# Performance work log

Measured on AMD Instinct MI355X. Metric: run time of the kernel, lower is better.

## Reference

```python
import jax, jax.numpy as jnp
import numpy as np
from jax import lax

C_IN, C_OUT, H, W = 64, 128, 512, 512


def setup_inputs() -> dict:
    key = jax.random.key(0)
    k1, k2, k3, k4 = jax.random.split(key, 4)
    x = jax.random.normal(k1, (C_IN, H, W), dtype=jnp.float32)
    # Conv2d params (eqx default: kernel 3x3, bias used). Small init scale for stability.
    conv_w = jax.random.normal(k2, (C_OUT, C_IN, 3, 3), dtype=jnp.float32) * 0.05
    conv_b = jax.random.normal(k3, (C_OUT,), dtype=jnp.float32) * 0.05
    fft_mask = jax.random.normal(k4, (C_OUT, H, W), dtype=jnp.float32)
    return {"x": x, "conv_w": conv_w, "conv_b": conv_b, "fft_mask": fft_mask}


def reference(x, conv_w, conv_b, fft_mask):
    # 3x3 same-padding conv on a single (C,H,W) sample -> (C_OUT,H,W)
    y = lax.conv_general_dilated(
        x[None],  # (1,C_IN,H,W)
        conv_w,
        window_strides=(1, 1),
        padding=((1, 1), (1, 1)),
        dimension_numbers=("NCHW", "OIHW", "NCHW"),
    )[0] + conv_b[:, None, None]
    # Per-channel spectral filter: FFT over (H,W), elementwise complex-mask
    # multiply, inverse FFT, take real part. Vectorized over channels.
    Y = jnp.fft.fftn(y, axes=(1, 2)) * fft_mask
    return jnp.fft.ifftn(Y, axes=(1, 2)).real
```

## Files before the change

### kernel.cpp

```cpp
#include <hip/hip_runtime.h>

#define CIN   64
#define COUT  128
#define HH    512
#define WW    512
#define HW    (HH*WW)

typedef __attribute__((ext_vector_type(8))) short  short8;
typedef __attribute__((ext_vector_type(4))) float  floatx4;


__device__ __forceinline__ unsigned short f2bf(float f) {
    unsigned u = __float_as_uint(f);
    u += 0x7fffu + ((u >> 16) & 1u);
    return (unsigned short)(u >> 16);
}


__global__ __launch_bounds__(256) void k_wprep(
        const float* __restrict__ cw,
        unsigned short* __restrict__ wt)
{
    int i = blockIdx.x * 256 + threadIdx.x;
    int tap = i >> 13;
    int co  = (i >> 6) & 127;
    int ci  = i & 63;
    wt[i] = f2bf(cw[(co * 64 + ci) * 9 + tap]);
}


__global__ __launch_bounds__(256) void k_xprep(
        const float* __restrict__ x,
        unsigned short* __restrict__ xt)
{
    __shared__ unsigned short tile[64][72];
    int t  = threadIdx.x;
    int h  = blockIdx.x >> 3;
    int w0 = (blockIdx.x & 7) << 6;
    int wl = t & 63;
#pragma unroll
    for (int it = 0; it < 16; ++it) {
        int ci = (t >> 6) + 4 * it;
        tile[wl][ci] = f2bf(x[ci * HW + h * 512 + w0 + wl]);
    }
    __syncthreads();
#pragma unroll
    for (int it = 0; it < 2; ++it) {
        int task = t + 256 * it;
        int w = task >> 3, seg = task & 7;
        *(short8*)&xt[((size_t)(h * 512 + w0 + w)) * 64 + seg * 8] =
            *(const short8*)&tile[w][seg * 8];
    }
}


__global__ __launch_bounds__(512) void k_conv(
        const unsigned short* __restrict__ xt,
        const unsigned short* __restrict__ wt,
        const float* __restrict__ bias,
        float* __restrict__ y)
{
    __shared__ __align__(16) unsigned short As[3][130][68];

    int b  = blockIdx.x;
    int h  = b >> 2;
    int w0 = (b & 3) << 7;
    int t  = threadIdx.x;
    int lane = t & 63, wv = t >> 6;
    int wm = wv >> 2, wn = wv & 3;
    int l15 = lane & 15, quad = lane >> 4;

    for (int idx = t; idx < 3 * 130 * 8; idx += 512) {
        int dy  = idx / 1040;
        int rem = idx - dy * 1040;
        int p   = rem >> 3, seg = rem & 7;
        int hp  = h + dy - 1;
        int wq  = w0 - 1 + p;
        short8 v = {0, 0, 0, 0, 0, 0, 0, 0};
        if ((unsigned)hp < 512u && (unsigned)wq < 512u)
            v = *(const short8*)&xt[((size_t)(hp * 512 + wq)) * 64 + seg * 8];
        *(short8*)&As[dy][p][seg * 8] = v;
    }
    __syncthreads();

    floatx4 acc[4][2];
#pragma unroll
    for (int mt = 0; mt < 4; ++mt)
#pragma unroll
        for (int nt = 0; nt < 2; ++nt) {
            floatx4 z = {0.f, 0.f, 0.f, 0.f};
            acc[mt][nt] = z;
        }

#pragma unroll
    for (int tap = 0; tap < 9; ++tap) {
        int dy = tap / 3, dx = tap - dy * 3;
        short8 bfr[2][2];
#pragma unroll
        for (int nt = 0; nt < 2; ++nt)
#pragma unroll
            for (int kc = 0; kc < 2; ++kc) {
                int co = wn * 32 + nt * 16 + l15;
                bfr[nt][kc] = *(const short8*)
                    &wt[(tap * 128 + co) * 64 + kc * 32 + quad * 8];
            }
#pragma unroll
        for (int kc = 0; kc < 2; ++kc) {
            int c0 = kc * 32 + quad * 8;
            short8 afr[4];
#pragma unroll
            for (int mt = 0; mt < 4; ++mt) {
                int row = wm * 64 + mt * 16 + l15 + dx;
                afr[mt] = *(const short8*)&As[dy][row][c0];
            }
#pragma unroll
            for (int mt = 0; mt < 4; ++mt)
#pragma unroll
                for (int nt = 0; nt < 2; ++nt)
                    acc[mt][nt] = __builtin_amdgcn_mfma_f32_16x16x32_bf16(
                        afr[mt], bfr[nt][kc], acc[mt][nt], 0, 0, 0);
        }
    }

#pragma unroll
    for (int nt = 0; nt < 2; ++nt) {
        int co = wn * 32 + nt * 16 + l15;
        float bv = bias[co];
#pragma unroll
        for (int mt = 0; mt < 4; ++mt) {
            floatx4 o = acc[mt][nt];
            o[0] += bv; o[1] += bv; o[2] += bv; o[3] += bv;
            int m = wm * 64 + mt * 16 + quad * 4;
            *(floatx4*)&y[co * HW + h * 512 + w0 + m] = o;
        }
    }
}


#define FS 576

template<int MODE>
__device__ __forceinline__ int slotf(int c, int a) {
    int m = a + (a >> 3);
    return (MODE == 0) ? c * FS + m
                       : m * 16 + c;
}

__device__ __forceinline__ float2 cadd(float2 a, float2 b){ return make_float2(a.x+b.x, a.y+b.y); }
__device__ __forceinline__ float2 csub(float2 a, float2 b){ return make_float2(a.x-b.x, a.y-b.y); }

template<int DIR> __device__ __forceinline__ float2 twmul(float2 a, float2 t){
    return (DIR > 0) ? make_float2(a.x*t.x - a.y*t.y, a.x*t.y + a.y*t.x)
                     : make_float2(a.x*t.x + a.y*t.y, a.y*t.x - a.x*t.y);
}
template<int DIR> __device__ __forceinline__ float2 mulJ(float2 a){
    return (DIR > 0) ? make_float2(a.y, -a.x) : make_float2(-a.y, a.x);
}

#define RSQRT2 0.70710678118654752f

template<int DIR> __device__ __forceinline__ void dft8(float2* x){
    float2 a0 = cadd(x[0], x[4]), b0 = csub(x[0], x[4]);
    float2 a1 = cadd(x[1], x[5]), b1 = csub(x[1], x[5]);
    float2 a2 = cadd(x[2], x[6]), b2 = csub(x[2], x[6]);
    float2 a3 = cadd(x[3], x[7]), b3 = csub(x[3], x[7]);
    b1 = (DIR > 0) ? make_float2((b1.x + b1.y)*RSQRT2, (b1.y - b1.x)*RSQRT2)
                   : make_float2((b1.x - b1.y)*RSQRT2, (b1.y + b1.x)*RSQRT2);
    b2 = mulJ<DIR>(b2);
    b3 = (DIR > 0) ? make_float2((b3.y - b3.x)*RSQRT2, -(b3.x + b3.y)*RSQRT2)
                   : make_float2(-(b3.x + b3.y)*RSQRT2, (b3.x - b3.y)*RSQRT2);
    float2 c0 = cadd(a0, a2), d0 = csub(a0, a2);
    float2 c1 = cadd(a1, a3), d1 = mulJ<DIR>(csub(a1, a3));
    x[0] = cadd(c0, c1); x[4] = csub(c0, c1);
    x[2] = cadd(d0, d1); x[6] = csub(d0, d1);
    float2 e0 = cadd(b0, b2), f0 = csub(b0, b2);
    float2 e1 = cadd(b1, b3), f1 = mulJ<DIR>(csub(b1, b3));
    x[1] = cadd(e0, e1); x[5] = csub(e0, e1);
    x[3] = cadd(f0, f1); x[7] = csub(f0, f1);
}

template<int MODE>
__device__ __forceinline__ void fft512_fwd(float2 X[4][8], float2* buf,
                                           const float2* tw, int w, int c) {
#pragma unroll
    for (int b = 0; b < 4; ++b) {
        dft8<1>(X[b]);
        int g = w + 16*b;
#pragma unroll
        for (int k = 1; k < 8; ++k) X[b][k] = twmul<1>(X[b][k], tw[g*k]);
    }
#pragma unroll
    for (int b = 0; b < 4; ++b) {
        int g = w + 16*b;
#pragma unroll
        for (int k = 0; k < 8; ++k) buf[slotf<MODE>(c, k*64 + g)] = X[b][k];
    }
    __syncthreads();
#pragma unroll
    for (int b = 0; b < 4; ++b) {
        int u = w + 16*b; int bs = (u >> 3)*64 + (u & 7);
#pragma unroll
        for (int g2 = 0; g2 < 8; ++g2) X[b][g2] = buf[slotf<MODE>(c, bs + 8*g2)];
    }
#pragma unroll
    for (int b = 0; b < 4; ++b) {
        dft8<1>(X[b]);
        int g1 = (w + 16*b) & 7;
#pragma unroll
        for (int k = 1; k < 8; ++k) X[b][k] = twmul<1>(X[b][k], tw[8*g1*k]);
    }
    __syncthreads();
#pragma unroll
    for (int b = 0; b < 4; ++b) {
        int u = w + 16*b; int bs = (u >> 3)*64 + (u & 7);
#pragma unroll
        for (int k = 0; k < 8; ++k) buf[slotf<MODE>(c, bs + 8*k)] = X[b][k];
    }
    __syncthreads();
#pragma unroll
    for (int b = 0; b < 4; ++b) {
        int v = w + 16*b;
#pragma unroll
        for (int g1 = 0; g1 < 8; ++g1) X[b][g1] = buf[slotf<MODE>(c, 8*v + g1)];
    }
#pragma unroll
    for (int b = 0; b < 4; ++b) dft8<1>(X[b]);
}

template<int MODE>
__device__ __forceinline__ void fft512_inv(float2 X[4][8], float2* buf,
                                           const float2* tw, int w, int c) {
#pragma unroll
    for (int b = 0; b < 4; ++b) dft8<-1>(X[b]);
    __syncthreads();
#pragma unroll
    for (int b = 0; b < 4; ++b) {
        int v = w + 16*b;
#pragma unroll
        for (int g1 = 0; g1 < 8; ++g1) buf[slotf<MODE>(c, 8*v + g1)] = X[b][g1];
    }
    __syncthreads();
#pragma unroll
    for (int b = 0; b < 4; ++b) {
        int u = w + 16*b; int bs = (u >> 3)*64 + (u & 7);
#pragma unroll
        for (int k = 0; k < 8; ++k) X[b][k] = buf[slotf<MODE>(c, bs + 8*k)];
    }
#pragma unroll
    for (int b = 0; b < 4; ++b) {
        int g1 = (w + 16*b) & 7;
#pragma unroll
        for (int k = 1; k < 8; ++k) X[b][k] = twmul<-1>(X[b][k], tw[8*g1*k]);
        dft8<-1>(X[b]);
    }
    __syncthreads();
#pragma unroll
    for (int b = 0; b < 4; ++b) {
        int u = w + 16*b; int bs = (u >> 3)*64 + (u & 7);
#pragma unroll
        for (int g2 = 0; g2 < 8; ++g2) buf[slotf<MODE>(c, bs + 8*g2)] = X[b][g2];
    }
    __syncthreads();
#pragma unroll
    for (int b = 0; b < 4; ++b) {
        int g = w + 16*b;
#pragma unroll
        for (int k = 0; k < 8; ++k) X[b][k] = buf[slotf<MODE>(c, k*64 + g)];
    }
#pragma unroll
    for (int b = 0; b < 4; ++b) {
        int g = w + 16*b;
#pragma unroll
        for (int k = 1; k < 8; ++k) X[b][k] = twmul<-1>(X[b][k], tw[g*k]);
        dft8<-1>(X[b]);
    }
}

__device__ __forceinline__ void build_tw(float2* tw, int t) {
    const float a0 = -6.283185307179586f / 512.0f;
    float s, c;
    __sincosf(a0 * (float)t, &s, &c);         tw[t]       = make_float2(c, s);
    __sincosf(a0 * (float)(t + 256), &s, &c); tw[t + 256] = make_float2(c, s);
}


__global__ __launch_bounds__(256) void k_rows_fwd_pair(
        const float* __restrict__ y,
        float2* __restrict__ Z)
{
    __shared__ float2 buf[16 * FS];
    __shared__ float2 tw[512];
    int t = threadIdx.x;
    build_tw(tw, t);
    int c = t >> 4, w = t & 15;
    int p = blockIdx.x >> 5, r0 = (blockIdx.x & 31) << 4;
    size_t baseA = (size_t)(2*p) * HW + (size_t)(r0 + c) * 512;
    size_t baseB = baseA + HW;

    float2 X[4][8];
#pragma unroll
    for (int b = 0; b < 4; ++b)
#pragma unroll
        for (int r = 0; r < 8; ++r) {
            int off = w + 16*b + 64*r;
            X[b][r] = make_float2(y[baseA + off], y[baseB + off]);
        }
    __syncthreads();
    fft512_fwd<0>(X, buf, tw, w, c);

    __syncthreads();
#pragma unroll
    for (int b = 0; b < 4; ++b) {
        int v = w + 16*b; int kb = (v >> 3) + 8*(v & 7);
#pragma unroll
        for (int m = 0; m < 8; ++m) buf[slotf<0>(c, kb + 64*m)] = X[b][m];
    }
    __syncthreads();
    size_t zbase = (size_t)p * HW + (size_t)r0 * 512;
    for (int it = 0; it < 32; ++it) {
        int n = t + 256*it; int row = n >> 9, col = n & 511;
        Z[zbase + (size_t)row*512 + col] = buf[slotf<0>(row, col)];
    }
}

__device__ __forceinline__ int col_of(int g, int j) {
    if (g == 0) return (j < 8) ? j : (j == 8 ? 256 : 496 + j);
    return (j < 8) ? 8*g + j : 512 - 8*g - 15 + j;
}
__device__ __forceinline__ int jmir(int g, int j) {
    return (g == 0) ? ((16 - j) & 15) : (15 - j);
}

__global__ __launch_bounds__(256) void k_cols_pair(
        float2* __restrict__ Z,
        const float* __restrict__ mask)
{
    __shared__ float2 buf[16 * FS];
    __shared__ float2 tw[512];
    int t = threadIdx.x;
    build_tw(tw, t);
    int c = t & 15, w = t >> 4;
    int p = blockIdx.x >> 5, g = blockIdx.x & 31;
    int colc = col_of(g, c);
    int colm = col_of(g, jmir(g, c));
    int cm   = jmir(g, c);
    size_t zch = (size_t)p * HW;
    size_t mA  = (size_t)(2*p) * HW;
    size_t mB  = mA + HW;

    float2 X[4][8];
#pragma unroll
    for (int b = 0; b < 4; ++b)
#pragma unroll
        for (int r = 0; r < 8; ++r)
            X[b][r] = Z[zch + (size_t)(w + 16*b + 64*r) * 512 + colc];
    __syncthreads();
    fft512_fwd<1>(X, buf, tw, w, c);

    __syncthreads();
#pragma unroll
    for (int b = 0; b < 4; ++b) {
        int v = w + 16*b; int kb = (v >> 3) + 8*(v & 7);
#pragma unroll
        for (int m = 0; m < 8; ++m) buf[slotf<1>(c, kb + 64*m)] = X[b][m];
    }
    __syncthreads();

    const float s4 = 0.25f / 262144.0f;
#pragma unroll
    for (int b = 0; b < 4; ++b) {
        int v = w + 16*b; int kb = (v >> 3) + 8*(v & 7);
#pragma unroll
        for (int m = 0; m < 8; ++m) {
            int k1  = kb + 64*m;
            int mk1 = (512 - k1) & 511;
            float2 P = X[b][m];
            float2 Q = buf[slotf<1>(cm, mk1)];
            float Mak = mask[mA + (size_t)k1  * 512 + colc];
            float Mbk = mask[mB + (size_t)k1  * 512 + colc];
            float Mam = mask[mA + (size_t)mk1 * 512 + colm];
            float Mbm = mask[mB + (size_t)mk1 * 512 + colm];
            float alpha = (Mak + Mam + Mbk + Mbm) * s4;
            float beta  = (Mak + Mam - Mbk - Mbm) * s4;
            X[b][m] = make_float2(alpha * P.x + beta * Q.x,
                                  alpha * P.y - beta * Q.y);
        }
    }
    fft512_inv<1>(X, buf, tw, w, c);

#pragma unroll
    for (int b = 0; b < 4; ++b)
#pragma unroll
        for (int r = 0; r < 8; ++r)
            Z[zch + (size_t)(w + 16*b + 64*r) * 512 + colc] = X[b][r];
}

__global__ __launch_bounds__(256) void k_rows_inv_pair(
        const float2* __restrict__ Z,
        float* __restrict__ out)
{
    __shared__ float2 buf[16 * FS];
    __shared__ float2 tw[512];
    int t = threadIdx.x;
    build_tw(tw, t);
    int c = t >> 4, w = t & 15;
    int p = blockIdx.x >> 5, r0 = (blockIdx.x & 31) << 4;
    size_t zbase = (size_t)p * HW + (size_t)r0 * 512;

    for (int it = 0; it < 32; ++it) {
        int n = t + 256*it; int row = n >> 9, col = n & 511;
        buf[slotf<0>(row, col)] = Z[zbase + (size_t)row*512 + col];
    }
    __syncthreads();

    float2 X[4][8];
#pragma unroll
    for (int b = 0; b < 4; ++b) {
        int v = w + 16*b; int kb = (v >> 3) + 8*(v & 7);
#pragma unroll
        for (int m = 0; m < 8; ++m) X[b][m] = buf[slotf<0>(c, kb + 64*m)];
    }
    fft512_inv<0>(X, buf, tw, w, c);

    size_t baseA = (size_t)(2*p) * HW + (size_t)(r0 + c) * 512;
    size_t baseB = baseA + HW;
#pragma unroll
    for (int b = 0; b < 4; ++b)
#pragma unroll
        for (int r = 0; r < 8; ++r) {
            int off = w + 16*b + 64*r;
            out[baseA + off] = X[b][r].x;
            out[baseB + off] = X[b][r].y;
        }
}


extern "C" void kernel_launch(void* const* d_in, const int* in_sizes, int n_in,
                              void* d_out, int out_size, void* d_ws, size_t ws_size,
                              hipStream_t stream) {
    const float* x    = (const float*)d_in[0];
    const float* cw   = (const float*)d_in[1];
    const float* cb   = (const float*)d_in[2];
    const float* mask = (const float*)d_in[3];

    float*  outRe = (float*)d_out;
    float2* Z     = (float2*)d_ws;

    unsigned short* xt = (unsigned short*)d_ws;
    unsigned short* wt = (unsigned short*)d_ws + (size_t)HW * 64;

    k_wprep<<<288, 256, 0, stream>>>(cw, wt);
    k_xprep<<<4096, 256, 0, stream>>>(x, xt);
    k_conv<<<2048, 512, 0, stream>>>(xt, wt, cb, outRe);
    k_rows_fwd_pair<<<2048, 256, 0, stream>>>(outRe, Z);
    k_cols_pair<<<2048, 256, 0, stream>>>(Z, mask);
    k_rows_inv_pair<<<2048, 256, 0, stream>>>(Z, outRe);
}
```

Measured before the change: 668.8 us.

## Store spectrum transposed, pre-transpose symmetrized mask, stage I/O through LDS

The intermediate spectrum is now stored column-major (transposed), so the column FFT pass reads and writes contiguous rows instead of strided columns. A new kernel transposes the mask and pre-adds it to its mirrored copy, writing into the output buffer as scratch, so the column kernel loads two coalesced values per element instead of four scattered ones. Row kernels stage their global loads and stores through LDS with float2 vectorized accesses, and the LDS slot mapping switches to an XOR swizzle to reduce bank conflicts. The cost is an extra mask-transpose pass over the full mask, plus additional LDS round trips and barriers.

```diff
diff --git a/kernel.cpp b/kernel.cpp
--- a/kernel.cpp
+++ b/kernel.cpp
@@ -50,6 +50,37 @@
         int w = task >> 3, seg = task & 7;
         *(short8*)&xt[((size_t)(h * 512 + w0 + w)) * 64 + seg * 8] =
             *(const short8*)&tile[w][seg * 8];
+    }
+}
+
+
+__global__ __launch_bounds__(256) void k_maskT2(
+        const float* __restrict__ mask,
+        float* __restrict__ mt)
+{
+    __shared__ float t1[64][65];
+    __shared__ float t2[64][65];
+    int b  = blockIdx.x;
+    int ch = b >> 6;
+    int k0 = ((b >> 3) & 7) << 6;
+    int c0 = (b & 7) << 6;
+    int t  = threadIdx.x;
+    int j  = t & 63, i0 = t >> 6;
+    const float* mch = mask + (size_t)ch * HW;
+#pragma unroll
+    for (int it = 0; it < 16; ++it) {
+        int i  = i0 + 4 * it;
+        int mi = (512 - (k0 + i)) & 511;
+        int mj = (512 - (c0 + j)) & 511;
+        t1[i][j] = mch[(size_t)(k0 + i) * 512 + (c0 + j)];
+        t2[i][j] = mch[(size_t)mi * 512 + mj];
+    }
+    __syncthreads();
+    float* och = mt + (size_t)ch * HW;
+#pragma unroll
+    for (int it = 0; it < 16; ++it) {
+        int jj = i0 + 4 * it;
+        och[(size_t)(c0 + jj) * 512 + k0 + j] = t1[j][jj] + t2[j][jj];
     }
 }
 
@@ -141,9 +172,8 @@
 
 template<int MODE>
 __device__ __forceinline__ int slotf(int c, int a) {
-    int m = a + (a >> 3);
-    return (MODE == 0) ? c * FS + m
-                       : m * 16 + c;
+    return (MODE == 0) ? c * FS + ((a + (a >> 3)) ^ c)
+                       : a * 16 + (c ^ (a & 15));
 }
 
 __device__ __forceinline__ float2 cadd(float2 a, float2 b){ return make_float2(a.x+b.x, a.y+b.y); }
@@ -294,17 +324,24 @@
     build_tw(tw, t);
     int c = t >> 4, w = t & 15;
     int p = blockIdx.x >> 5, r0 = (blockIdx.x & 31) << 4;
-    size_t baseA = (size_t)(2*p) * HW + (size_t)(r0 + c) * 512;
-    size_t baseB = baseA + HW;
-
+    const float* yA = y + (size_t)(2*p) * HW;
+    const float* yB = yA + HW;
+
+    for (int it = 0; it < 16; ++it) {
+        int n = t + 256*it;
+        int rr = n >> 8, q = n & 255;
+        float2 a2 = *(const float2*)&yA[(size_t)(r0 + rr)*512 + 2*q];
+        float2 b2 = *(const float2*)&yB[(size_t)(r0 + rr)*512 + 2*q];
+        buf[slotf<0>(rr, 2*q)]     = make_float2(a2.x, b2.x);
+        buf[slotf<0>(rr, 2*q + 1)] = make_float2(a2.y, b2.y);
+    }
+    __syncthreads();
     float2 X[4][8];
 #pragma unroll
     for (int b = 0; b < 4; ++b)
 #pragma unroll
-        for (int r = 0; r < 8; ++r) {
-            int off = w + 16*b + 64*r;
-            X[b][r] = make_float2(y[baseA + off], y[baseB + off]);
-        }
+        for (int r = 0; r < 8; ++r)
+            X[b][r] = buf[slotf<0>(c, w + 16*b + 64*r)];
     __syncthreads();
     fft512_fwd<0>(X, buf, tw, w, c);
 
@@ -316,10 +353,11 @@
         for (int m = 0; m < 8; ++m) buf[slotf<0>(c, kb + 64*m)] = X[b][m];
     }
     __syncthreads();
-    size_t zbase = (size_t)p * HW + (size_t)r0 * 512;
+    size_t zb = (size_t)p * HW + r0;
     for (int it = 0; it < 32; ++it) {
-        int n = t + 256*it; int row = n >> 9, col = n & 511;
-        Z[zbase + (size_t)row*512 + col] = buf[slotf<0>(row, col)];
+        int n = t + 256*it;
+        int col = n >> 4, rr = n & 15;
+        Z[zb + (size_t)col*512 + rr] = buf[slotf<0>(rr, col)];
     }
 }
 
@@ -333,27 +371,43 @@
 
 __global__ __launch_bounds__(256) void k_cols_pair(
         float2* __restrict__ Z,
-        const float* __restrict__ mask)
-{
-    __shared__ float2 buf[16 * FS];
+        const float* __restrict__ mt)
+{
+    __shared__ float2 buf[8192];
     __shared__ float2 tw[512];
     int t = threadIdx.x;
     build_tw(tw, t);
     int c = t & 15, w = t >> 4;
     int p = blockIdx.x >> 5, g = blockIdx.x & 31;
     int colc = col_of(g, c);
-    int colm = col_of(g, jmir(g, c));
     int cm   = jmir(g, c);
     size_t zch = (size_t)p * HW;
-    size_t mA  = (size_t)(2*p) * HW;
-    size_t mB  = mA + HW;
-
+    const float* mAp = mt + (size_t)(2*p) * HW + (size_t)colc * 512;
+    const float* mBp = mAp + HW;
+
+    for (int it = 0; it < 32; ++it) {
+        int n = t + 256*it;
+        int cj = n >> 9, row = n & 511;
+        buf[slotf<1>(cj, row)] = Z[zch + (size_t)col_of(g, cj)*512 + row];
+    }
+    float Sa[4][8], Sb[4][8];
+#pragma unroll
+    for (int b = 0; b < 4; ++b) {
+        int v = w + 16*b; int kb = (v >> 3) + 8*(v & 7);
+#pragma unroll
+        for (int m = 0; m < 8; ++m) {
+            int k1 = kb + 64*m;
+            Sa[b][m] = mAp[k1];
+            Sb[b][m] = mBp[k1];
+        }
+    }
+    __syncthreads();
     float2 X[4][8];
 #pragma unroll
     for (int b = 0; b < 4; ++b)
 #pragma unroll
         for (int r = 0; r < 8; ++r)
-            X[b][r] = Z[zch + (size_t)(w + 16*b + 64*r) * 512 + colc];
+            X[b][r] = buf[slotf<1>(c, w + 16*b + 64*r)];
     __syncthreads();
     fft512_fwd<1>(X, buf, tw, w, c);
 
@@ -376,23 +430,25 @@
             int mk1 = (512 - k1) & 511;
             float2 P = X[b][m];
             float2 Q = buf[slotf<1>(cm, mk1)];
-            float Mak = mask[mA + (size_t)k1  * 512 + colc];
-            float Mbk = mask[mB + (size_t)k1  * 512 + colc];
-            float Mam = mask[mA + (size_t)mk1 * 512 + colm];
-            float Mbm = mask[mB + (size_t)mk1 * 512 + colm];
-            float alpha = (Mak + Mam + Mbk + Mbm) * s4;
-            float beta  = (Mak + Mam - Mbk - Mbm) * s4;
+            float alpha = (Sa[b][m] + Sb[b][m]) * s4;
+            float beta  = (Sa[b][m] - Sb[b][m]) * s4;
             X[b][m] = make_float2(alpha * P.x + beta * Q.x,
                                   alpha * P.y - beta * Q.y);
         }
     }
     fft512_inv<1>(X, buf, tw, w, c);
-
+    __syncthreads();
 #pragma unroll
     for (int b = 0; b < 4; ++b)
 #pragma unroll
         for (int r = 0; r < 8; ++r)
-            Z[zch + (size_t)(w + 16*b + 64*r) * 512 + colc] = X[b][r];
+            buf[slotf<1>(c, w + 16*b + 64*r)] = X[b][r];
+    __syncthreads();
+    for (int it = 0; it < 32; ++it) {
+        int n = t + 256*it;
+        int cj = n >> 9, row = n & 511;
+        Z[zch + (size_t)col_of(g, cj)*512 + row] = buf[slotf<1>(cj, row)];
+    }
 }
 
 __global__ __launch_bounds__(256) void k_rows_inv_pair(
@@ -405,11 +461,12 @@
     build_tw(tw, t);
     int c = t >> 4, w = t & 15;
     int p = blockIdx.x >> 5, r0 = (blockIdx.x & 31) << 4;
-    size_t zbase = (size_t)p * HW + (size_t)r0 * 512;
+    size_t zb = (size_t)p * HW + r0;
 
     for (int it = 0; it < 32; ++it) {
-        int n = t + 256*it; int row = n >> 9, col = n & 511;
-        buf[slotf<0>(row, col)] = Z[zbase + (size_t)row*512 + col];
+        int n = t + 256*it;
+        int col = n >> 4, rr = n & 15;
+        buf[slotf<0>(rr, col)] = Z[zb + (size_t)col*512 + rr];
     }
     __syncthreads();
 
@@ -421,17 +478,23 @@
         for (int m = 0; m < 8; ++m) X[b][m] = buf[slotf<0>(c, kb + 64*m)];
     }
     fft512_inv<0>(X, buf, tw, w, c);
-
-    size_t baseA = (size_t)(2*p) * HW + (size_t)(r0 + c) * 512;
-    size_t baseB = baseA + HW;
+    __syncthreads();
 #pragma unroll
     for (int b = 0; b < 4; ++b)
 #pragma unroll
-        for (int r = 0; r < 8; ++r) {
-            int off = w + 16*b + 64*r;
-            out[baseA + off] = X[b][r].x;
-            out[baseB + off] = X[b][r].y;
-        }
+        for (int r = 0; r < 8; ++r)
+            buf[slotf<0>(c, w + 16*b + 64*r)] = X[b][r];
+    __syncthreads();
+    float* oA = out + (size_t)(2*p) * HW;
+    float* oB = oA + HW;
+    for (int it = 0; it < 16; ++it) {
+        int n = t + 256*it;
+        int rr = n >> 8, q = n & 255;
+        float2 v0 = buf[slotf<0>(rr, 2*q)];
+        float2 v1 = buf[slotf<0>(rr, 2*q + 1)];
+        *(float2*)&oA[(size_t)(r0 + rr)*512 + 2*q] = make_float2(v0.x, v1.x);
+        *(float2*)&oB[(size_t)(r0 + rr)*512 + 2*q] = make_float2(v0.y, v1.y);
+    }
 }
 
 
@@ -444,7 +507,7 @@
     const float* mask = (const float*)d_in[3];
 
     float*  outRe = (float*)d_out;
-    float2* Z     = (float2*)d_ws;
+    float2* ZT    = (float2*)d_ws;
 
     unsigned short* xt = (unsigned short*)d_ws;
     unsigned short* wt = (unsigned short*)d_ws + (size_t)HW * 64;
@@ -452,7 +515,8 @@
     k_wprep<<<288, 256, 0, stream>>>(cw, wt);
     k_xprep<<<4096, 256, 0, stream>>>(x, xt);
     k_conv<<<2048, 512, 0, stream>>>(xt, wt, cb, outRe);
-    k_rows_fwd_pair<<<2048, 256, 0, stream>>>(outRe, Z);
-    k_cols_pair<<<2048, 256, 0, stream>>>(Z, mask);
-    k_rows_inv_pair<<<2048, 256, 0, stream>>>(Z, outRe);
-}
+    k_rows_fwd_pair<<<2048, 256, 0, stream>>>(outRe, ZT);
+    k_maskT2<<<8192, 256, 0, stream>>>(mask, outRe);
+    k_cols_pair<<<2048, 256, 0, stream>>>(ZT, outRe);
+    k_rows_inv_pair<<<2048, 256, 0, stream>>>(ZT, outRe);
+}
```

Result: faster. 652.8 us (-2.4%).
